# Kernel tuning notes

Measured on AMD Instinct MI355X. Metric: run time of the kernel, lower is better.

Reference implementation:

```python
import jax, jax.numpy as jnp
import numpy as np

D_MODEL = 2048
NHEAD = 32
GROUPS = 8
HEAD_DIM = D_MODEL // NHEAD  # 64
HPG = NHEAD // GROUPS        # heads per group = 4
ROPE_BASE = 10000.0


def _rope(x):
    # x: [B, H, S, D] -- rotate-half RoPE over full head dim, matching RoPE module
    S, D = x.shape[2], x.shape[3]
    theta = 1.0 / (ROPE_BASE ** (jnp.arange(0, D, 2, dtype=jnp.float32) / D))  # [D/2]
    idx_theta = jnp.arange(S, dtype=jnp.float32)[:, None] * theta[None, :]     # [S, D/2]
    ang = jnp.concatenate([idx_theta, idx_theta], axis=-1)                     # [S, D]
    cos = jnp.cos(ang)[None, None]  # [1,1,S,D]
    sin = jnp.sin(ang)[None, None]
    d2 = D // 2
    neg_half = jnp.concatenate([-x[..., d2:], x[..., :d2]], axis=-1)
    return x * cos + neg_half * sin


def setup_inputs() -> dict:
    key = jax.random.key(0)
    ks = jax.random.split(key, 9)
    B, S = 2, 2048
    s_in = 1.0 / np.sqrt(D_MODEL)
    return {
        "x": jax.random.normal(ks[0], (B, S, D_MODEL), jnp.float32),
        "Wq": jax.random.normal(ks[1], (D_MODEL, D_MODEL), jnp.float32) * s_in,
        "bq": jax.random.normal(ks[2], (D_MODEL,), jnp.float32) * 0.01,
        "Wk": jax.random.normal(ks[3], (HEAD_DIM * GROUPS, D_MODEL), jnp.float32) * s_in,
        "bk": jax.random.normal(ks[4], (HEAD_DIM * GROUPS,), jnp.float32) * 0.01,
        "Wv": jax.random.normal(ks[5], (HEAD_DIM * GROUPS, D_MODEL), jnp.float32) * s_in,
        "bv": jax.random.normal(ks[6], (HEAD_DIM * GROUPS,), jnp.float32) * 0.01,
        "Wo": jax.random.normal(ks[7], (D_MODEL, D_MODEL), jnp.float32) * s_in,
        "bo": jax.random.normal(ks[8], (D_MODEL,), jnp.float32) * 0.01,
    }


def reference(x, Wq, bq, Wk, bk, Wv, bv, Wo, bo):
    B, S, _ = x.shape
    # projections (torch Linear: x @ W.T + b)
    q = (x @ Wq.T + bq).reshape(B, S, NHEAD, HEAD_DIM).transpose(0, 2, 1, 3)   # [B,H,S,D]
    k = (x @ Wk.T + bk).reshape(B, S, GROUPS, HEAD_DIM).transpose(0, 2, 1, 3)  # [B,G,S,D]
    v = (x @ Wv.T + bv).reshape(B, S, GROUPS, HEAD_DIM).transpose(0, 2, 1, 3)  # [B,G,S,D]
    q = _rope(q)
    k = _rope(k)
    # grouped-query attention: share each k/v group across HPG query heads
    qg = q.reshape(B, GROUPS, HPG, S, HEAD_DIM)
    scale = 1.0 / np.sqrt(HEAD_DIM)
    scores = jnp.einsum('bghsd,bgtd->bghst', qg, k) * scale  # [B,G,Hpg,S,S]
    causal = jnp.tril(jnp.ones((S, S), dtype=bool))
    scores = jnp.where(causal, scores, jnp.finfo(scores.dtype).min)
    attn = jax.nn.softmax(scores, axis=-1)
    out = jnp.einsum('bghst,bgtd->bghsd', attn, v)           # [B,G,Hpg,S,D]
    out = out.reshape(B, NHEAD, S, HEAD_DIM).transpose(0, 2, 1, 3).reshape(B, S, D_MODEL)
    return out @ Wo.T + bo
```

## Files before the change

kernel.cpp:

```cpp
#include <hip/hip_runtime.h>

typedef unsigned short u16;
typedef __bf16 bf16x8 __attribute__((ext_vector_type(8)));
typedef float floatx4 __attribute__((ext_vector_type(4)));
typedef u16 u16x8 __attribute__((ext_vector_type(8)));
typedef u16 u16x4 __attribute__((ext_vector_type(4)));

#define D_MODEL 2048
#define S_LEN   2048
#define BATCH   2
#define NHEAD   32
#define GROUPS  8
#define HEAD_DIM 64
#define KV_DIM  512

__device__ __forceinline__ float bf2f(u16 h) {
  unsigned int u = ((unsigned int)h) << 16;
  return __builtin_bit_cast(float, u);
}
__device__ __forceinline__ u16 f2bf(float f) {
  unsigned int u = __builtin_bit_cast(unsigned int, f);
  u += 0x7fffu + ((u >> 16) & 1u);
  return (u16)(u >> 16);
}
__device__ __forceinline__ float fexp2(float x) {
  float r;
  asm("v_exp_f32 %0, %1" : "=v"(r) : "v"(x));
  return r;
}

#define GLD_LDS(gp, lp) \
  __builtin_amdgcn_global_load_lds((__attribute__((address_space(1))) void*)(gp), \
                                   (__attribute__((address_space(3))) void*)(lp), 16, 0, 0)

__global__ __launch_bounds__(256)
void cvt5_f32_bf16(const float* s0, const float* s1, const float* s2,
                   const float* s3, const float* s4,
                   u16* d0, u16* d1, u16* d2, u16* d3, u16* d4,
                   int n0, int n1, int n2, int n3, int n4,
                   float* ct, float* st)
{
  if (blockIdx.y == 5) {
    int idx = blockIdx.x * 256 + threadIdx.x;
    if (idx < S_LEN * 32) {
      int s = idx >> 5, d = idx & 31;
      float theta = __expf(-(float)d * 0.28782313662425574f);
      float sn, cs;
      sincosf((float)s * theta, &sn, &cs);
      ct[idx] = cs; st[idx] = sn;
    }
    return;
  }
  const float* s; u16* d; int n;
  switch (blockIdx.y) {
    case 0: s = s0; d = d0; n = n0; break;
    case 1: s = s1; d = d1; n = n1; break;
    case 2: s = s2; d = d2; n = n2; break;
    case 3: s = s3; d = d3; n = n3; break;
    default: s = s4; d = d4; n = n4; break;
  }
  long i = ((long)blockIdx.x * 256 + threadIdx.x) * 8;
  if (i >= n) return;
  floatx4 a = *(const floatx4*)(s + i);
  floatx4 b = *(const floatx4*)(s + i + 4);
  u16x8 r;
#pragma unroll
  for (int j = 0; j < 4; ++j) { r[j] = f2bf(a[j]); r[4 + j] = f2bf(b[j]); }
  *(u16x8*)(d + i) = r;
}

__global__ __launch_bounds__(256, 3)
void gemm_qkv(const u16* __restrict__ A, const u16* __restrict__ Wq,
              const u16* __restrict__ Wkv,
              const float* __restrict__ bq, const float* __restrict__ bk,
              const float* __restrict__ bv,
              u16* __restrict__ Qb, u16* __restrict__ Kb, u16* __restrict__ Vt,
              const float* __restrict__ ct, const float* __restrict__ st)
{
  const int K = D_MODEL;
  __shared__ __align__(16) u16 As[2 * 128 * 32];
  __shared__ __align__(16) u16 Bs[2 * 128 * 32];
  const int t = threadIdx.x;
  const int w = t >> 6, l = t & 63;
  const int lr = l & 15, lq = l >> 4;
  const int wm = (w >> 1) * 64, wn = (w & 1) * 64;
  const long bm = (long)blockIdx.x * 128;

  const bool isQ = blockIdx.y < 16;
  const long bn = isQ ? (long)blockIdx.y * 128 : (long)(blockIdx.y - 16) * 128;
  const u16* W = isQ ? Wq : Wkv;

  floatx4 acc[4][4] = {};

  const u16* a0 = A + (bm + (t >> 2)) * (long)K + (t & 3) * 8;
  const u16* a1 = a0 + 64L * K;
  const u16* pB0 = W + (bn + (t >> 2)) * (long)K + (t & 3) * 8;
  const u16* pB1 = pB0 + 64L * K;
  u16* As0 = As + w * 512;
  u16* As1 = As + 2048 + w * 512;
  u16* Bs0 = Bs + w * 512;
  u16* Bs1 = Bs + 2048 + w * 512;

  for (int k0 = 0; k0 < K; k0 += 64) {
    GLD_LDS(a0 + k0, As0);
    GLD_LDS(a1 + k0, As1);
    GLD_LDS(pB0 + k0, Bs0);
    GLD_LDS(pB1 + k0, Bs1);
    GLD_LDS(a0 + k0 + 32, As0 + 4096);
    GLD_LDS(a1 + k0 + 32, As1 + 4096);
    GLD_LDS(pB0 + k0 + 32, Bs0 + 4096);
    GLD_LDS(pB1 + k0 + 32, Bs1 + 4096);
    __syncthreads();

#pragma unroll
    for (int kk = 0; kk < 2; ++kk) {
      const u16* as = As + kk * 4096;
      const u16* bs = Bs + kk * 4096;
      bf16x8 av[4], bv8[4];
#pragma unroll
      for (int i = 0; i < 4; ++i)
        av[i] = *(const bf16x8*)(as + (wm + i * 16 + lr) * 32 + lq * 8);
#pragma unroll
      for (int j = 0; j < 4; ++j)
        bv8[j] = *(const bf16x8*)(bs + (wn + j * 16 + lr) * 32 + lq * 8);
#pragma unroll
      for (int i = 0; i < 4; ++i)
#pragma unroll
        for (int j = 0; j < 4; ++j)
          acc[i][j] = __builtin_amdgcn_mfma_f32_16x16x32_bf16(av[i], bv8[j], acc[i][j], 0, 0, 0);
    }
    __syncthreads();
  }

  if (isQ || bn < KV_DIM) {
    const float* bias = isQ ? bq : bk;
    u16* dst = isQ ? Qb : Kb;
    const long ldc = isQ ? D_MODEL : KV_DIM;
    float bb[4];
#pragma unroll
    for (int j = 0; j < 4; ++j)
      bb[j] = bias[bn + wn + j * 16 + lr];
#pragma unroll
    for (int i = 0; i < 4; ++i) {
#pragma unroll
      for (int rr = 0; rr < 4; ++rr) {
        long row = bm + wm + i * 16 + lq * 4 + rr;
        int srow = (int)row & (S_LEN - 1);
        float c0 = ct[srow * 32 + lr],      sn0 = st[srow * 32 + lr];
        float c1 = ct[srow * 32 + 16 + lr], sn1 = st[srow * 32 + 16 + lr];
        float v0 = acc[i][0][rr] + bb[0];
        float v1 = acc[i][1][rr] + bb[1];
        float v2 = acc[i][2][rr] + bb[2];
        float v3 = acc[i][3][rr] + bb[3];
        u16* cp = dst + row * ldc + bn + wn + lr;
        cp[0]  = f2bf(v0 * c0 - v2 * sn0);
        cp[16] = f2bf(v1 * c1 - v3 * sn1);
        cp[32] = f2bf(v2 * c0 + v0 * sn0);
        cp[48] = f2bf(v3 * c1 + v1 * sn1);
      }
    }
  } else {
    float bb[4];
#pragma unroll
    for (int j = 0; j < 4; ++j)
      bb[j] = bv[bn - KV_DIM + wn + j * 16 + lr];
#pragma unroll
    for (int i = 0; i < 4; ++i) {
      int row0 = (int)bm + wm + i * 16 + lq * 4;
      int b = row0 >> 11, s0r = row0 & (S_LEN - 1);
#pragma unroll
      for (int j = 0; j < 4; ++j) {
        int vcol = (int)bn - KV_DIM + wn + j * 16 + lr;
        u16x4 pv;
#pragma unroll
        for (int rr = 0; rr < 4; ++rr)
          pv[rr] = f2bf(acc[i][j][rr] + bb[j]);
        *(u16x4*)(Vt + ((long)b * KV_DIM + vcol) * S_LEN + s0r) = pv;
      }
    }
  }
}

__global__ __launch_bounds__(256, 3)
void gemm_out(const u16* __restrict__ A, const u16* __restrict__ W,
              const float* __restrict__ bias, float* __restrict__ C,
              int K, int ldc)
{
  __shared__ __align__(16) u16 As[2 * 128 * 32];
  __shared__ __align__(16) u16 Bs[2 * 128 * 32];
  const int t = threadIdx.x;
  const int w = t >> 6, l = t & 63;
  const int lr = l & 15, lq = l >> 4;
  const int wm = (w >> 1) * 64, wn = (w & 1) * 64;
  const long bm = (long)blockIdx.x * 128;
  const long bn = (long)blockIdx.y * 128;

  floatx4 acc[4][4] = {};

  const u16* a0 = A + (bm + (t >> 2)) * (long)K + (t & 3) * 8;
  const u16* a1 = a0 + 64L * K;
  const u16* pB0 = W + (bn + (t >> 2)) * (long)K + (t & 3) * 8;
  const u16* pB1 = pB0 + 64L * K;
  u16* As0 = As + w * 512;
  u16* As1 = As + 2048 + w * 512;
  u16* Bs0 = Bs + w * 512;
  u16* Bs1 = Bs + 2048 + w * 512;

  for (int k0 = 0; k0 < K; k0 += 64) {
    GLD_LDS(a0 + k0, As0);
    GLD_LDS(a1 + k0, As1);
    GLD_LDS(pB0 + k0, Bs0);
    GLD_LDS(pB1 + k0, Bs1);
    GLD_LDS(a0 + k0 + 32, As0 + 4096);
    GLD_LDS(a1 + k0 + 32, As1 + 4096);
    GLD_LDS(pB0 + k0 + 32, Bs0 + 4096);
    GLD_LDS(pB1 + k0 + 32, Bs1 + 4096);
    __syncthreads();

#pragma unroll
    for (int kk = 0; kk < 2; ++kk) {
      const u16* as = As + kk * 4096;
      const u16* bs = Bs + kk * 4096;
      bf16x8 av[4], bv[4];
#pragma unroll
      for (int i = 0; i < 4; ++i)
        av[i] = *(const bf16x8*)(as + (wm + i * 16 + lr) * 32 + lq * 8);
#pragma unroll
      for (int j = 0; j < 4; ++j)
        bv[j] = *(const bf16x8*)(bs + (wn + j * 16 + lr) * 32 + lq * 8);
#pragma unroll
      for (int i = 0; i < 4; ++i)
#pragma unroll
        for (int j = 0; j < 4; ++j)
          acc[i][j] = __builtin_amdgcn_mfma_f32_16x16x32_bf16(av[i], bv[j], acc[i][j], 0, 0, 0);
    }
    __syncthreads();
  }

  float bb[4];
#pragma unroll
  for (int j = 0; j < 4; ++j)
    bb[j] = bias[bn + wn + j * 16 + lr];
#pragma unroll
  for (int i = 0; i < 4; ++i) {
#pragma unroll
    for (int rr = 0; rr < 4; ++rr) {
      long row = bm + wm + i * 16 + lq * 4 + rr;
      long cidx = row * (long)ldc + bn + wn + lr;
      float* cp = C + cidx;
#pragma unroll
      for (int j = 0; j < 4; ++j)
        cp[j * 16] = acc[i][j][rr] + bb[j];
    }
  }
}

__global__ __launch_bounds__(512, 4)
void gqa_attn(const u16* Q, const u16* __restrict__ Kc,
              const u16* __restrict__ Vt, u16* O)
{
  __shared__ __align__(16) u16 KV[2][16 * 512];
  __shared__ __align__(16) u16 Ps[8][2][16 * 72];

  const int pr = blockIdx.x;
  const int bh = blockIdx.y;
  const int b = bh >> 5, h = bh & 31, g = h >> 2;

  const int t = threadIdx.x;
  const int w = t >> 6, l = t & 63;
  const int w4 = w & 3;
  const int lr = l & 15, lq = l >> 4;

  const int qt = (w < 4) ? pr : (15 - pr);
  const int NKTw = 2 * qt + 2;
  const int NKTmax = 32 - 2 * pr;

  const u16* Kp = Kc + ((long)b * S_LEN) * KV_DIM + g * HEAD_DIM;
  const u16* Vp = Vt + ((long)b * KV_DIM + g * HEAD_DIM) * S_LEN;
  const u16* Qp = Q + ((long)b * S_LEN + qt * 128) * D_MODEL + h * HEAD_DIM;
  u16* Op = O + ((long)b * S_LEN + qt * 128) * D_MODEL + h * HEAD_DIM;

  const bool isK = (w < 4);
  long sb[2];
  {
    const int sig2 = ((l >> 2) ^ (l >> 4)) & 1;
    const int sig1 = ((l >> 1) ^ (l >> 3)) & 1;
    const int sig0 = (l ^ sig2) & 1;
    const int row = ((l >> 2) & 14) | sig2;
    const int cl = ((sig1 << 1) | sig0) * 8;
#pragma unroll
    for (int q = 0; q < 2; ++q) {
      sb[q] = isK ? ((long)(w4 * 16 + row) * KV_DIM + q * 32 + cl)
                  : ((long)(w4 * 16 + row) * S_LEN + q * 32 + cl);
    }
  }
  const u16* sp = isK ? Kp : Vp;
  const long smul = isK ? (long)64 * KV_DIM : 64;
  const int dbase = (isK ? 0 : 4096) + w4 * 1024;
  const int koff = ((4 * lr + lq) ^ (lr & 7)) * 8;

  bf16x8 onesf;
#pragma unroll
  for (int e = 0; e < 8; ++e) onesf[e] = (__bf16)1.0f;

#define STAGE(bufi, kt_) do { \
    const long soff_ = (long)(kt_) * smul; \
    GLD_LDS(sp + soff_ + sb[0], &KV[bufi][dbase + 0 * 512]); \
    GLD_LDS(sp + soff_ + sb[1], &KV[bufi][dbase + 1 * 512]); \
  } while (0)

  bf16x8 qf00, qf01, qf10, qf11;
  {
    const u16* qr0 = Qp + (long)(w4 * 16 + lr) * D_MODEL;
    qf00 = *(const bf16x8*)(qr0 + lq * 8);
    qf01 = *(const bf16x8*)(qr0 + 32 + lq * 8);
    const u16* qr1 = qr0 + (long)64 * D_MODEL;
    qf10 = *(const bf16x8*)(qr1 + lq * 8);
    qf11 = *(const bf16x8*)(qr1 + 32 + lq * 8);
  }

  floatx4 o0[4] = {}, o1[4] = {};
  floatx4 lsa0 = {}, lsa1 = {};

  STAGE(0, 0);
#pragma unroll 1
  for (int kt = 0; kt < NKTmax; ++kt) {
    __syncthreads();
    if (kt + 1 < NKTmax) STAGE((kt + 1) & 1, kt + 1);
    if (kt >= NKTw) continue;

    const bool D0 = (kt == NKTw - 2);
    const bool D1 = (kt == NKTw - 1);
    const u16* buf_ = &KV[kt & 1][0];

    floatx4 z0[4] = {}, z1[4] = {};
#pragma unroll
    for (int j = 0; j < 4; ++j) {
      bf16x8 kf0 = *(const bf16x8*)(buf_ + j * 1024 + koff);
      bf16x8 kf1 = *(const bf16x8*)(buf_ + j * 1024 + 512 + koff);
      if (!D1 && (!D0 || j <= w4)) {
        z0[j] = __builtin_amdgcn_mfma_f32_16x16x32_bf16(kf0, qf00, z0[j], 0, 0, 0);
        z0[j] = __builtin_amdgcn_mfma_f32_16x16x32_bf16(kf1, qf01, z0[j], 0, 0, 0);
      }
      if (!D1 || j <= w4) {
        z1[j] = __builtin_amdgcn_mfma_f32_16x16x32_bf16(kf0, qf10, z1[j], 0, 0, 0);
        z1[j] = __builtin_amdgcn_mfma_f32_16x16x32_bf16(kf1, qf11, z1[j], 0, 0, 0);
      }
    }

    if (!D1) {
#pragma unroll
      for (int j = 0; j < 4; ++j) {
        u16x4 pk;
#pragma unroll
        for (int rr = 0; rr < 4; ++rr) {
          float ps = fexp2(z0[j][rr] * 0.18033688011112042f - 23.083120654223414f);
          if (D0 && (j * 16 + lq * 4 + rr > w4 * 16 + lr)) ps = 0.f;
          pk[rr] = __builtin_bit_cast(u16, (__bf16)ps);
        }
        *(u16x4*)&Ps[w][0][lr * 72 + j * 16 + lq * 4] = pk;
      }
    }
#pragma unroll
    for (int j = 0; j < 4; ++j) {
      u16x4 pk;
#pragma unroll
      for (int rr = 0; rr < 4; ++rr) {
        float ps = fexp2(z1[j][rr] * 0.18033688011112042f - 23.083120654223414f);
        if (D1 && (j * 16 + lq * 4 + rr > w4 * 16 + lr)) ps = 0.f;
        pk[rr] = __builtin_bit_cast(u16, (__bf16)ps);
      }
      *(u16x4*)&Ps[w][1][lr * 72 + j * 16 + lq * 4] = pk;
    }

    bf16x8 pa00 = *(const bf16x8*)&Ps[w][0][lr * 72 + lq * 8];
    bf16x8 pa01 = *(const bf16x8*)&Ps[w][0][lr * 72 + 32 + lq * 8];
    bf16x8 pa10 = *(const bf16x8*)&Ps[w][1][lr * 72 + lq * 8];
    bf16x8 pa11 = *(const bf16x8*)&Ps[w][1][lr * 72 + 32 + lq * 8];

    if (!D1) {
      lsa0 = __builtin_amdgcn_mfma_f32_16x16x32_bf16(pa00, onesf, lsa0, 0, 0, 0);
      if (!D0 || w4 >= 2)
        lsa0 = __builtin_amdgcn_mfma_f32_16x16x32_bf16(pa01, onesf, lsa0, 0, 0, 0);
    }
    lsa1 = __builtin_amdgcn_mfma_f32_16x16x32_bf16(pa10, onesf, lsa1, 0, 0, 0);
    if (!D1 || w4 >= 2)
      lsa1 = __builtin_amdgcn_mfma_f32_16x16x32_bf16(pa11, onesf, lsa1, 0, 0, 0);

    const u16* vbuf_ = buf_ + 4096;
#pragma unroll
    for (int j = 0; j < 4; ++j) {
      bf16x8 vb0 = *(const bf16x8*)(vbuf_ + j * 1024 + koff);
      bf16x8 vb1 = *(const bf16x8*)(vbuf_ + j * 1024 + 512 + koff);
      if (!D1) {
        o0[j] = __builtin_amdgcn_mfma_f32_16x16x32_bf16(pa00, vb0, o0[j], 0, 0, 0);
        if (!D0 || w4 >= 2)
          o0[j] = __builtin_amdgcn_mfma_f32_16x16x32_bf16(pa01, vb1, o0[j], 0, 0, 0);
      }
      o1[j] = __builtin_amdgcn_mfma_f32_16x16x32_bf16(pa10, vb0, o1[j], 0, 0, 0);
      if (!D1 || w4 >= 2)
        o1[j] = __builtin_amdgcn_mfma_f32_16x16x32_bf16(pa11, vb1, o1[j], 0, 0, 0);
    }
  }
#undef STAGE

#pragma unroll
  for (int s = 0; s < 2; ++s) {
    const floatx4 lsv = s ? lsa1 : lsa0;
    const floatx4* oo = s ? o1 : o0;
#pragma unroll
    for (int rr = 0; rr < 4; ++rr) {
      float inv = 1.f / lsv[rr];
      long row = s * 64 + w4 * 16 + lq * 4 + rr;
      u16* op = Op + row * (long)D_MODEL + lr;
#pragma unroll
      for (int j = 0; j < 4; ++j)
        op[j * 16] = f2bf(oo[j][rr] * inv);
    }
  }
}

extern "C" void kernel_launch(void* const* d_in, const int* in_sizes, int n_in,
                              void* d_out, int out_size, void* d_ws, size_t ws_size,
                              hipStream_t stream)
{
  const float* x  = (const float*)d_in[0];
  const float* Wq = (const float*)d_in[1];
  const float* bq = (const float*)d_in[2];
  const float* Wk = (const float*)d_in[3];
  const float* bk = (const float*)d_in[4];
  const float* Wv = (const float*)d_in[5];
  const float* bv = (const float*)d_in[6];
  const float* Wo = (const float*)d_in[7];
  const float* bo = (const float*)d_in[8];
  float* out = (float*)d_out;

  const int Sx  = BATCH * S_LEN * D_MODEL;
  const int SWq = D_MODEL * D_MODEL;
  const int SWk = KV_DIM * D_MODEL;
  const int SWv = KV_DIM * D_MODEL;
  const int SWo = D_MODEL * D_MODEL;

  u16* xb  = (u16*)d_ws;
  u16* Wqb = xb  + Sx;
  u16* Wkb = Wqb + SWq;
  u16* Wvb = Wkb + SWk;
  u16* Wob = Wvb + SWv;
  u16* Qb  = Wob + SWo;
  u16* Kb  = Qb + (size_t)4096 * 2048;
  u16* Vtb = Kb + (size_t)4096 * 512;
  float* ctab = (float*)(Vtb + (size_t)BATCH * KV_DIM * S_LEN);
  float* stab = ctab + S_LEN * 32;
  u16* AO  = Qb;

  const int M = BATCH * S_LEN;
  dim3 blk(256);
  cvt5_f32_bf16<<<dim3(4096, 6), blk, 0, stream>>>(x, Wq, Wk, Wv, Wo,
                                                   xb, Wqb, Wkb, Wvb, Wob,
                                                   Sx, SWq, SWk, SWv, SWo,
                                                   ctab, stab);
  gemm_qkv<<<dim3(M / 128, 24), blk, 0, stream>>>(xb, Wqb, Wkb, bq, bk, bv,
                                                  Qb, Kb, Vtb, ctab, stab);
  gqa_attn<<<dim3(8, BATCH * NHEAD), dim3(512), 0, stream>>>(Qb, Kb, Vtb, AO);
  gemm_out<<<dim3(M / 128, D_MODEL / 128), blk, 0, stream>>>(AO, Wob, bo, out, D_MODEL, D_MODEL);
}
```

Baseline: 289.9 us.

## Process both paired query tiles per wave to share K/V fragment loads

The attention kernel moves from 512 threads, where wave halves handled the two paired query tiles separately, to 256 threads where each wave processes both tiles (pr and 15-pr). Each K/V fragment read from LDS now feeds MFMAs for both tiles, which halves LDS fragment reads per unit of work, and each wave issues twice as many staging loads. In exchange, registers per wave roughly double (two sets of accumulators, Q fragments and scores), so occupancy may drop. Per-wave serial work also grows, which could leave the GPU less latency hiding.

```diff
diff --git a/kernel.cpp b/kernel.cpp
--- a/kernel.cpp
+++ b/kernel.cpp
@@ -255,12 +255,12 @@
   }
 }
 
-__global__ __launch_bounds__(512, 4)
+__global__ __launch_bounds__(256, 2)
 void gqa_attn(const u16* Q, const u16* __restrict__ Kc,
               const u16* __restrict__ Vt, u16* O)
 {
   __shared__ __align__(16) u16 KV[2][16 * 512];
-  __shared__ __align__(16) u16 Ps[8][2][16 * 72];
+  __shared__ __align__(16) u16 Ps[4][2][16 * 72];
 
   const int pr = blockIdx.x;
   const int bh = blockIdx.y;
@@ -268,20 +268,12 @@
 
   const int t = threadIdx.x;
   const int w = t >> 6, l = t & 63;
-  const int w4 = w & 3;
   const int lr = l & 15, lq = l >> 4;
-
-  const int qt = (w < 4) ? pr : (15 - pr);
-  const int NKTw = 2 * qt + 2;
-  const int NKTmax = 32 - 2 * pr;
 
   const u16* Kp = Kc + ((long)b * S_LEN) * KV_DIM + g * HEAD_DIM;
   const u16* Vp = Vt + ((long)b * KV_DIM + g * HEAD_DIM) * S_LEN;
-  const u16* Qp = Q + ((long)b * S_LEN + qt * 128) * D_MODEL + h * HEAD_DIM;
-  u16* Op = O + ((long)b * S_LEN + qt * 128) * D_MODEL + h * HEAD_DIM;
-
-  const bool isK = (w < 4);
-  long sb[2];
+
+  long sb[4];
   {
     const int sig2 = ((l >> 2) ^ (l >> 4)) & 1;
     const int sig1 = ((l >> 1) ^ (l >> 3)) & 1;
@@ -289,14 +281,16 @@
     const int row = ((l >> 2) & 14) | sig2;
     const int cl = ((sig1 << 1) | sig0) * 8;
 #pragma unroll
-    for (int q = 0; q < 2; ++q) {
-      sb[q] = isK ? ((long)(w4 * 16 + row) * KV_DIM + q * 32 + cl)
-                  : ((long)(w4 * 16 + row) * S_LEN + q * 32 + cl);
-    }
-  }
-  const u16* sp = isK ? Kp : Vp;
-  const long smul = isK ? (long)64 * KV_DIM : 64;
-  const int dbase = (isK ? 0 : 4096) + w4 * 1024;
+    for (int q = 0; q < 4; ++q) {
+      const int r = (w & 1) * 4 + q;
+      const int jj = r >> 1, cc = r & 1;
+      sb[q] = (w < 2) ? ((long)(jj * 16 + row) * KV_DIM + cc * 32 + cl)
+                      : ((long)(jj * 16 + row) * S_LEN + cc * 32 + cl);
+    }
+  }
+  const u16* sp = (w < 2) ? Kp : Vp;
+  const long smul = (w < 2) ? (long)64 * KV_DIM : 64;
+  const int dbase = ((w < 2) ? 0 : 4096) + (w & 1) * 2048;
   const int koff = ((4 * lr + lq) ^ (lr & 7)) * 8;
 
   bf16x8 onesf;
@@ -307,115 +301,140 @@
     const long soff_ = (long)(kt_) * smul; \
     GLD_LDS(sp + soff_ + sb[0], &KV[bufi][dbase + 0 * 512]); \
     GLD_LDS(sp + soff_ + sb[1], &KV[bufi][dbase + 1 * 512]); \
+    GLD_LDS(sp + soff_ + sb[2], &KV[bufi][dbase + 2 * 512]); \
+    GLD_LDS(sp + soff_ + sb[3], &KV[bufi][dbase + 3 * 512]); \
   } while (0)
 
-  bf16x8 qf00, qf01, qf10, qf11;
-  {
-    const u16* qr0 = Qp + (long)(w4 * 16 + lr) * D_MODEL;
-    qf00 = *(const bf16x8*)(qr0 + lq * 8);
-    qf01 = *(const bf16x8*)(qr0 + 32 + lq * 8);
-    const u16* qr1 = qr0 + (long)64 * D_MODEL;
-    qf10 = *(const bf16x8*)(qr1 + lq * 8);
-    qf11 = *(const bf16x8*)(qr1 + 32 + lq * 8);
-  }
-
-  floatx4 o0[4] = {}, o1[4] = {};
-  floatx4 lsa0 = {}, lsa1 = {};
+  const int qtp[2] = {pr, 15 - pr};
+  const int NA = 2 * pr + 2;
+  const int NB = 32 - 2 * pr;
+
+  bf16x8 qf[2][2][2];
+#pragma unroll
+  for (int p = 0; p < 2; ++p) {
+    const u16* Qp = Q + ((long)b * S_LEN + qtp[p] * 128) * D_MODEL + h * HEAD_DIM;
+#pragma unroll
+    for (int s = 0; s < 2; ++s) {
+      const u16* qr = Qp + (long)(s * 64 + w * 16 + lr) * D_MODEL;
+      qf[p][s][0] = *(const bf16x8*)(qr + lq * 8);
+      qf[p][s][1] = *(const bf16x8*)(qr + 32 + lq * 8);
+    }
+  }
+
+  floatx4 o[2][2][4] = {};
+  floatx4 lsa[2][2] = {};
 
   STAGE(0, 0);
 #pragma unroll 1
-  for (int kt = 0; kt < NKTmax; ++kt) {
+  for (int kt = 0; kt < NB; ++kt) {
     __syncthreads();
-    if (kt + 1 < NKTmax) STAGE((kt + 1) & 1, kt + 1);
-    if (kt >= NKTw) continue;
-
-    const bool D0 = (kt == NKTw - 2);
-    const bool D1 = (kt == NKTw - 1);
+    if (kt + 1 < NB) STAGE((kt + 1) & 1, kt + 1);
     const u16* buf_ = &KV[kt & 1][0];
-
-    floatx4 z0[4] = {}, z1[4] = {};
+    const bool actA = (kt < NA);
+    const bool d0p[2] = {kt == NA - 2, kt == NB - 2};
+    const bool d1p[2] = {kt == NA - 1, kt == NB - 1};
+
+    floatx4 z[2][2][4] = {};
 #pragma unroll
     for (int j = 0; j < 4; ++j) {
       bf16x8 kf0 = *(const bf16x8*)(buf_ + j * 1024 + koff);
       bf16x8 kf1 = *(const bf16x8*)(buf_ + j * 1024 + 512 + koff);
-      if (!D1 && (!D0 || j <= w4)) {
-        z0[j] = __builtin_amdgcn_mfma_f32_16x16x32_bf16(kf0, qf00, z0[j], 0, 0, 0);
-        z0[j] = __builtin_amdgcn_mfma_f32_16x16x32_bf16(kf1, qf01, z0[j], 0, 0, 0);
-      }
-      if (!D1 || j <= w4) {
-        z1[j] = __builtin_amdgcn_mfma_f32_16x16x32_bf16(kf0, qf10, z1[j], 0, 0, 0);
-        z1[j] = __builtin_amdgcn_mfma_f32_16x16x32_bf16(kf1, qf11, z1[j], 0, 0, 0);
-      }
-    }
-
-    if (!D1) {
+#pragma unroll
+      for (int p = 0; p < 2; ++p) {
+        if (p == 0 && !actA) continue;
+        const bool D0 = d0p[p], D1 = d1p[p];
+        if (!D1 && (!D0 || j <= w)) {
+          z[p][0][j] = __builtin_amdgcn_mfma_f32_16x16x32_bf16(kf0, qf[p][0][0], z[p][0][j], 0, 0, 0);
+          z[p][0][j] = __builtin_amdgcn_mfma_f32_16x16x32_bf16(kf1, qf[p][0][1], z[p][0][j], 0, 0, 0);
+        }
+        if (!D1 || j <= w) {
+          z[p][1][j] = __builtin_amdgcn_mfma_f32_16x16x32_bf16(kf0, qf[p][1][0], z[p][1][j], 0, 0, 0);
+          z[p][1][j] = __builtin_amdgcn_mfma_f32_16x16x32_bf16(kf1, qf[p][1][1], z[p][1][j], 0, 0, 0);
+        }
+      }
+    }
+
+    bf16x8 pa[2][2][2];
+#pragma unroll
+    for (int p = 0; p < 2; ++p) {
+      if (p == 0 && !actA) continue;
+      const bool D0 = d0p[p], D1 = d1p[p];
+      if (!D1) {
+#pragma unroll
+        for (int j = 0; j < 4; ++j) {
+          u16x4 pk;
+#pragma unroll
+          for (int rr = 0; rr < 4; ++rr) {
+            float ps = fexp2(z[p][0][j][rr] * 0.18033688011112042f - 23.083120654223414f);
+            if (D0 && (j * 16 + lq * 4 + rr > w * 16 + lr)) ps = 0.f;
+            pk[rr] = __builtin_bit_cast(u16, (__bf16)ps);
+          }
+          *(u16x4*)&Ps[w][0][lr * 72 + j * 16 + lq * 4] = pk;
+        }
+      }
 #pragma unroll
       for (int j = 0; j < 4; ++j) {
         u16x4 pk;
 #pragma unroll
         for (int rr = 0; rr < 4; ++rr) {
-          float ps = fexp2(z0[j][rr] * 0.18033688011112042f - 23.083120654223414f);
-          if (D0 && (j * 16 + lq * 4 + rr > w4 * 16 + lr)) ps = 0.f;
+          float ps = fexp2(z[p][1][j][rr] * 0.18033688011112042f - 23.083120654223414f);
+          if (D1 && (j * 16 + lq * 4 + rr > w * 16 + lr)) ps = 0.f;
           pk[rr] = __builtin_bit_cast(u16, (__bf16)ps);
         }
-        *(u16x4*)&Ps[w][0][lr * 72 + j * 16 + lq * 4] = pk;
-      }
-    }
-#pragma unroll
-    for (int j = 0; j < 4; ++j) {
-      u16x4 pk;
-#pragma unroll
-      for (int rr = 0; rr < 4; ++rr) {
-        float ps = fexp2(z1[j][rr] * 0.18033688011112042f - 23.083120654223414f);
-        if (D1 && (j * 16 + lq * 4 + rr > w4 * 16 + lr)) ps = 0.f;
-        pk[rr] = __builtin_bit_cast(u16, (__bf16)ps);
-      }
-      *(u16x4*)&Ps[w][1][lr * 72 + j * 16 + lq * 4] = pk;
-    }
-
-    bf16x8 pa00 = *(const bf16x8*)&Ps[w][0][lr * 72 + lq * 8];
-    bf16x8 pa01 = *(const bf16x8*)&Ps[w][0][lr * 72 + 32 + lq * 8];
-    bf16x8 pa10 = *(const bf16x8*)&Ps[w][1][lr * 72 + lq * 8];
-    bf16x8 pa11 = *(const bf16x8*)&Ps[w][1][lr * 72 + 32 + lq * 8];
-
-    if (!D1) {
-      lsa0 = __builtin_amdgcn_mfma_f32_16x16x32_bf16(pa00, onesf, lsa0, 0, 0, 0);
-      if (!D0 || w4 >= 2)
-        lsa0 = __builtin_amdgcn_mfma_f32_16x16x32_bf16(pa01, onesf, lsa0, 0, 0, 0);
-    }
-    lsa1 = __builtin_amdgcn_mfma_f32_16x16x32_bf16(pa10, onesf, lsa1, 0, 0, 0);
-    if (!D1 || w4 >= 2)
-      lsa1 = __builtin_amdgcn_mfma_f32_16x16x32_bf16(pa11, onesf, lsa1, 0, 0, 0);
+        *(u16x4*)&Ps[w][1][lr * 72 + j * 16 + lq * 4] = pk;
+      }
+      pa[p][0][0] = *(const bf16x8*)&Ps[w][0][lr * 72 + lq * 8];
+      pa[p][0][1] = *(const bf16x8*)&Ps[w][0][lr * 72 + 32 + lq * 8];
+      pa[p][1][0] = *(const bf16x8*)&Ps[w][1][lr * 72 + lq * 8];
+      pa[p][1][1] = *(const bf16x8*)&Ps[w][1][lr * 72 + 32 + lq * 8];
+
+      if (!D1) {
+        lsa[p][0] = __builtin_amdgcn_mfma_f32_16x16x32_bf16(pa[p][0][0], onesf, lsa[p][0], 0, 0, 0);
+        if (!D0 || w >= 2)
+          lsa[p][0] = __builtin_amdgcn_mfma_f32_16x16x32_bf16(pa[p][0][1], onesf, lsa[p][0], 0, 0, 0);
+      }
+      lsa[p][1] = __builtin_amdgcn_mfma_f32_16x16x32_bf16(pa[p][1][0], onesf, lsa[p][1], 0, 0, 0);
+      if (!D1 || w >= 2)
+        lsa[p][1] = __builtin_amdgcn_mfma_f32_16x16x32_bf16(pa[p][1][1], onesf, lsa[p][1], 0, 0, 0);
+    }
 
     const u16* vbuf_ = buf_ + 4096;
 #pragma unroll
     for (int j = 0; j < 4; ++j) {
       bf16x8 vb0 = *(const bf16x8*)(vbuf_ + j * 1024 + koff);
       bf16x8 vb1 = *(const bf16x8*)(vbuf_ + j * 1024 + 512 + koff);
-      if (!D1) {
-        o0[j] = __builtin_amdgcn_mfma_f32_16x16x32_bf16(pa00, vb0, o0[j], 0, 0, 0);
-        if (!D0 || w4 >= 2)
-          o0[j] = __builtin_amdgcn_mfma_f32_16x16x32_bf16(pa01, vb1, o0[j], 0, 0, 0);
-      }
-      o1[j] = __builtin_amdgcn_mfma_f32_16x16x32_bf16(pa10, vb0, o1[j], 0, 0, 0);
-      if (!D1 || w4 >= 2)
-        o1[j] = __builtin_amdgcn_mfma_f32_16x16x32_bf16(pa11, vb1, o1[j], 0, 0, 0);
+#pragma unroll
+      for (int p = 0; p < 2; ++p) {
+        if (p == 0 && !actA) continue;
+        const bool D0 = d0p[p], D1 = d1p[p];
+        if (!D1) {
+          o[p][0][j] = __builtin_amdgcn_mfma_f32_16x16x32_bf16(pa[p][0][0], vb0, o[p][0][j], 0, 0, 0);
+          if (!D0 || w >= 2)
+            o[p][0][j] = __builtin_amdgcn_mfma_f32_16x16x32_bf16(pa[p][0][1], vb1, o[p][0][j], 0, 0, 0);
+        }
+        o[p][1][j] = __builtin_amdgcn_mfma_f32_16x16x32_bf16(pa[p][1][0], vb0, o[p][1][j], 0, 0, 0);
+        if (!D1 || w >= 2)
+          o[p][1][j] = __builtin_amdgcn_mfma_f32_16x16x32_bf16(pa[p][1][1], vb1, o[p][1][j], 0, 0, 0);
+      }
     }
   }
 #undef STAGE
 
 #pragma unroll
-  for (int s = 0; s < 2; ++s) {
-    const floatx4 lsv = s ? lsa1 : lsa0;
-    const floatx4* oo = s ? o1 : o0;
-#pragma unroll
-    for (int rr = 0; rr < 4; ++rr) {
-      float inv = 1.f / lsv[rr];
-      long row = s * 64 + w4 * 16 + lq * 4 + rr;
-      u16* op = Op + row * (long)D_MODEL + lr;
-#pragma unroll
-      for (int j = 0; j < 4; ++j)
-        op[j * 16] = f2bf(oo[j][rr] * inv);
+  for (int p = 0; p < 2; ++p) {
+    u16* Op = O + ((long)b * S_LEN + qtp[p] * 128) * D_MODEL + h * HEAD_DIM;
+#pragma unroll
+    for (int s = 0; s < 2; ++s) {
+      const floatx4 lsv = lsa[p][s];
+#pragma unroll
+      for (int rr = 0; rr < 4; ++rr) {
+        float inv = 1.f / lsv[rr];
+        long row = s * 64 + w * 16 + lq * 4 + rr;
+        u16* op = Op + row * (long)D_MODEL + lr;
+#pragma unroll
+        for (int j = 0; j < 4; ++j)
+          op[j * 16] = f2bf(o[p][s][j][rr] * inv);
+      }
     }
   }
 }
@@ -461,6 +480,6 @@
                                                    ctab, stab);
   gemm_qkv<<<dim3(M / 128, 24), blk, 0, stream>>>(xb, Wqb, Wkb, bq, bk, bv,
                                                   Qb, Kb, Vtb, ctab, stab);
-  gqa_attn<<<dim3(8, BATCH * NHEAD), dim3(512), 0, stream>>>(Qb, Kb, Vtb, AO);
+  gqa_attn<<<dim3(8, BATCH * NHEAD), blk, 0, stream>>>(Qb, Kb, Vtb, AO);
   gemm_out<<<dim3(M / 128, D_MODEL / 128), blk, 0, stream>>>(AO, Wob, bo, out, D_MODEL, D_MODEL);
 }
```

Measured after the change: 293.8 us. Within noise of the previous version (+1.3%).
